# Kernel optimization log

Measured on AMD Instinct MI355X. Metric: run time of the kernel, lower is better.

The kernel has to match this reference:

```python
import jax, jax.numpy as jnp
import numpy as np

EPS = 1e-5
NORM_EPS = 1e-12  # torch F.normalize eps
HEADS = 8


def _ln(x, w, b):
    # channel LayerNorm on NCHW: normalize over C (axis 1), population var
    mu = x.mean(axis=1, keepdims=True)
    var = x.var(axis=1, keepdims=True)
    return (x - mu) / jnp.sqrt(var + EPS) * w[None, :, None, None] + b[None, :, None, None]


def _conv1x1(x, w):
    # x: (B,C,H,W), w: (O,C)
    return jnp.einsum('bchw,oc->bohw', x, w)


def _dwconv3x3(x, w):
    # depthwise 3x3, w: (C,1,3,3)
    C = x.shape[1]
    return jax.lax.conv_general_dilated(
        x, w, window_strides=(1, 1), padding='SAME',
        feature_group_count=C, dimension_numbers=('NCHW', 'OIHW', 'NCHW'))


def _l2norm(v):
    n = jnp.linalg.norm(v, axis=-1, keepdims=True)
    return v / jnp.maximum(n, NORM_EPS)


def setup_inputs() -> dict:
    key = jax.random.key(0)
    ks = jax.random.split(key, 12)
    dim, hid = 128, 512  # hidden_dim = dim * 4
    B, H, W = 8, 128, 128
    s = 0.05
    return {
        'x': jax.random.normal(ks[0], (B, dim, H, W), jnp.float32),
        'ln1_w': jnp.ones((dim,), jnp.float32),
        'ln1_b': jnp.zeros((dim,), jnp.float32),
        'wq': jax.random.normal(ks[1], (dim, dim), jnp.float32) * s,
        'wk': jax.random.normal(ks[2], (dim, dim), jnp.float32) * s,
        'wv': jax.random.normal(ks[3], (dim, dim), jnp.float32) * s,
        'dwq': jax.random.normal(ks[4], (dim, 1, 3, 3), jnp.float32) * s,
        'dwk': jax.random.normal(ks[5], (dim, 1, 3, 3), jnp.float32) * s,
        'dwv': jax.random.normal(ks[6], (dim, 1, 3, 3), jnp.float32) * s,
        'temp': jnp.ones((HEADS, 1, 1), jnp.float32),
        'wo': jax.random.normal(ks[7], (dim, dim), jnp.float32) * s,
        'ln2_w': jnp.ones((dim,), jnp.float32),
        'ln2_b': jnp.zeros((dim,), jnp.float32),
        'w_in': jax.random.normal(ks[8], (2 * hid, dim), jnp.float32) * s,
        'dw_ffn': jax.random.normal(ks[9], (2 * hid, 1, 3, 3), jnp.float32) * s,
        'w_out': jax.random.normal(ks[10], (dim, hid), jnp.float32) * s,
    }


def reference(x, ln1_w, ln1_b, wq, wk, wv, dwq, dwk, dwv, temp, wo,
              ln2_w, ln2_b, w_in, dw_ffn, w_out):
    B, C, H, W = x.shape
    d = C // HEADS

    # ---- MDTA channel attention ----
    xn = _ln(x, ln1_w, ln1_b)
    q = _dwconv3x3(_conv1x1(xn, wq), dwq).reshape(B, HEADS, d, H * W)
    k = _dwconv3x3(_conv1x1(xn, wk), dwk).reshape(B, HEADS, d, H * W)
    v = _dwconv3x3(_conv1x1(xn, wv), dwv).reshape(B, HEADS, d, H * W)
    q = _l2norm(q)
    k = _l2norm(k)
    attn = jnp.einsum('bhdn,bhen->bhde', q, k) * temp[None]  # (B,h,d,d)
    attn = jax.nn.softmax(attn, axis=-1)
    out = jnp.einsum('bhde,bhen->bhdn', attn, v).reshape(B, C, H, W)
    x = x + _conv1x1(out, wo)

    # ---- GEGLU FFN with depthwise conv ----
    yn = _ln(x, ln2_w, ln2_b)
    y = _dwconv3x3(_conv1x1(yn, w_in), dw_ffn)
    y1, y2 = jnp.split(y, 2, axis=1)
    y = jax.nn.gelu(y1, approximate=False) * y2
    return x + _conv1x1(y, w_out)
```

## Files before the change

### kernel.cpp

```cpp
#include <hip/hip_runtime.h>
#include <hip/hip_bf16.h>
#include <type_traits>

using bf16 = __hip_bfloat16;
using f32x4  = __attribute__((ext_vector_type(4))) float;
using bf16x8 = __attribute__((ext_vector_type(8))) short;

constexpr int NPIX = 16384;
constexpr int CDIM = 128;

constexpr size_t OFF_MU    = 0;
constexpr size_t OFF_RSTD  = 524288;
constexpr size_t OFF_MU2   = 1048576;
constexpr size_t OFF_RSTD2 = 1572864;
constexpr size_t OFF_SSQ   = 2097152;
constexpr size_t OFF_S     = 2105344;
constexpr size_t OFF_DWP   = 2170880;
constexpr size_t OFF_WQKVB = 2184704;
constexpr size_t OFF_WINB  = 2283008;
constexpr size_t OFF_WOUTB = 2545152;
constexpr size_t OFF_WEFFB = 2676224;
constexpr size_t OFF_X2B   = 2938368;
constexpr size_t OFF_QKV   = 36492800;
constexpr size_t OFF_QKVDW = 137156096;
constexpr size_t OFF_G     = 36492800;
constexpr size_t OFF_Y     = 170710528;

__device__ inline float ldf(const float* p) { return *p; }
__device__ inline float ldf(const bf16* p) { return __bfloat162float(*p); }

__global__ void pack_w(const float* __restrict__ wq, const float* __restrict__ wk,
                       const float* __restrict__ wv, const float* __restrict__ dwq,
                       const float* __restrict__ dwk, const float* __restrict__ dwv,
                       const float* __restrict__ w_in, const float* __restrict__ wout,
                       bf16* __restrict__ Wqkvb, float* __restrict__ dwp,
                       bf16* __restrict__ winb, bf16* __restrict__ woutb) {
    int i = blockIdx.x * 256 + threadIdx.x;
    if (i < 384 * 128) {
        int r = i >> 7, c = i & 127;
        float v = (r < 128) ? wq[r * 128 + c] : (r < 256) ? wk[(r - 128) * 128 + c]
                                                          : wv[(r - 256) * 128 + c];
        Wqkvb[i] = __float2bfloat16(v);
    }
    if (i < 384 * 9) {
        int r = i / 9, j = i % 9;
        dwp[i] = (r < 128) ? dwq[r * 9 + j] : (r < 256) ? dwk[(r - 128) * 9 + j]
                                                        : dwv[(r - 256) * 9 + j];
    }
    if (i < 1024 * 128) winb[i] = __float2bfloat16(w_in[i]);
    if (i < 128 * 512)  woutb[i] = __float2bfloat16(wout[i]);
}

template <typename XT>
__global__ __launch_bounds__(256) void ln_stats(const XT* __restrict__ X, size_t xBs,
                                                float* __restrict__ mu,
                                                float* __restrict__ rstd) {
    const int b = blockIdx.y;
    const XT* Xb = X + (size_t)b * xBs;
    int n = blockIdx.x * 256 + threadIdx.x;
    float s = 0.f, s2 = 0.f;
    for (int c = 0; c < CDIM; ++c) {
        float v = ldf(&Xb[(size_t)c * NPIX + n]);
        s += v; s2 += v * v;
    }
    float m = s * (1.f / CDIM);
    float var = s2 * (1.f / CDIM) - m * m;
    mu[b * NPIX + n] = m;
    rstd[b * NPIX + n] = rsqrtf(var + 1e-5f);
}

template <typename XT, typename OT, typename RT, bool LN, bool RES>
__global__ __launch_bounds__(256) void gemm_mfma(
    const bf16* __restrict__ Wb0, int wBs, const XT* __restrict__ X0, size_t xBs,
    const float* __restrict__ mu0, const float* __restrict__ rstd0,
    const float* __restrict__ lnw, const float* __restrict__ lnb,
    const RT* __restrict__ res0, size_t rBs, OT* __restrict__ out0, size_t oBs, int K) {
    __shared__ bf16 Wl[64][40];
    __shared__ bf16 Xt[128][40];
    const int t = threadIdx.x;
    const int b = blockIdx.z;
    const bf16* Wb = Wb0 + (size_t)b * wBs;
    const XT* X = X0 + (size_t)b * xBs;
    const RT* res = RES ? res0 + (size_t)b * rBs : nullptr;
    OT* out = out0 + (size_t)b * oBs;
    const float* mu = LN ? mu0 + (size_t)b * NPIX : nullptr;
    const float* rstd = LN ? rstd0 + (size_t)b * NPIX : nullptr;

    const int lane = t & 63, wave = t >> 6;
    const int wm = wave >> 1, wn = wave & 1;
    const int g = lane >> 4, lr = lane & 15;
    const int m0 = blockIdx.x * 64, n0 = blockIdx.y * 128;

    const int sw_row = t >> 2, sw_k8 = (t & 3) * 8;
    const int sx_n = t & 127, sx_kh = t >> 7;

    float x_mu = 0.f, x_rs = 0.f;
    if constexpr (LN) { x_mu = mu[n0 + sx_n]; x_rs = rstd[n0 + sx_n]; }

    f32x4 acc[2][4];
    #pragma unroll
    for (int i = 0; i < 2; ++i)
        #pragma unroll
        for (int j = 0; j < 4; ++j)
            acc[i][j] = (f32x4){0.f, 0.f, 0.f, 0.f};

    for (int kc = 0; kc < K; kc += 32) {
        uint4 wv = *(const uint4*)(Wb + (size_t)(m0 + sw_row) * K + kc + sw_k8);
        *(uint4*)&Wl[sw_row][sw_k8] = wv;
        {
            union { uint4 u[2]; bf16 h[16]; } T;
            const int kb = kc + sx_kh * 16;
            #pragma unroll
            for (int kk = 0; kk < 16; ++kk) {
                float v = ldf(&X[(size_t)(kb + kk) * NPIX + n0 + sx_n]);
                if constexpr (LN) v = (v - x_mu) * x_rs * lnw[kb + kk] + lnb[kb + kk];
                T.h[kk] = __float2bfloat16(v);
            }
            *(uint4*)&Xt[sx_n][sx_kh * 16] = T.u[0];
            *(uint4*)&Xt[sx_n][sx_kh * 16 + 8] = T.u[1];
        }
        __syncthreads();
        bf16x8 af[2], bfr[4];
        #pragma unroll
        for (int i = 0; i < 2; ++i)
            af[i] = *(const bf16x8*)&Wl[wm * 32 + i * 16 + lr][g * 8];
        #pragma unroll
        for (int j = 0; j < 4; ++j)
            bfr[j] = *(const bf16x8*)&Xt[wn * 64 + j * 16 + lr][g * 8];
        #pragma unroll
        for (int i = 0; i < 2; ++i)
            #pragma unroll
            for (int j = 0; j < 4; ++j)
                acc[i][j] = __builtin_amdgcn_mfma_f32_16x16x32_bf16(af[i], bfr[j], acc[i][j], 0, 0, 0);
        __syncthreads();
    }
    #pragma unroll
    for (int i = 0; i < 2; ++i) {
        #pragma unroll
        for (int j = 0; j < 4; ++j) {
            #pragma unroll
            for (int r = 0; r < 4; ++r) {
                int row = m0 + wm * 32 + i * 16 + g * 4 + r;
                int col = n0 + wn * 64 + j * 16 + lr;
                float v = acc[i][j][r];
                if constexpr (RES) v += ldf(&res[(size_t)row * NPIX + col]);
                if constexpr (std::is_same_v<OT, float>)
                    out[(size_t)row * NPIX + col] = v;
                else
                    out[(size_t)row * NPIX + col] = __float2bfloat16(v);
            }
        }
    }
}

__global__ __launch_bounds__(256) void dwconv_qkv(const bf16* __restrict__ in0,
                                                  bf16* __restrict__ out0,
                                                  const float* __restrict__ w9,
                                                  float* __restrict__ ssq0) {
    const int b = blockIdx.y, c = blockIdx.x;
    const bf16* in = in0 + ((size_t)b * 384 + c) * NPIX;
    bf16* out = out0 + ((size_t)b * 384 + c) * NPIX;
    float* ssq = ssq0 + b * 256;
    const int t = threadIdx.x;
    const int lane = t & 63;
    const int tx = t & 15, ty = t >> 4;
    const int x0 = tx * 8, ybase = ty * 8;
    float w[9];
    #pragma unroll
    for (int j = 0; j < 9; ++j) w[j] = w9[c * 9 + j];

    float r[3][10];
    auto loadrow = [&](int yy, float* d) {
        union { uint4 u; bf16 h[8]; } V;
        bool ok = (yy >= 0 && yy <= 127);
        V.u = ok ? *(const uint4*)(in + yy * 128 + x0) : make_uint4(0u, 0u, 0u, 0u);
        #pragma unroll
        for (int j = 0; j < 8; ++j) d[j + 1] = __bfloat162float(V.h[j]);
        float Lv = __shfl(d[8], lane - 1, 64);
        float Rv = __shfl(d[1], lane + 1, 64);
        d[0] = (tx == 0) ? 0.f : Lv;
        d[9] = (tx == 15) ? 0.f : Rv;
    };

    loadrow(ybase - 1, r[0]);
    loadrow(ybase, r[1]);
    float s2 = 0.f;
    #pragma unroll
    for (int j = 0; j < 8; ++j) {
        loadrow(ybase + j + 1, r[(j + 2) % 3]);
        const float* rm = r[j % 3];
        const float* rc = r[(j + 1) % 3];
        const float* rp = r[(j + 2) % 3];
        union { uint4 u; bf16 h[8]; } O;
        #pragma unroll
        for (int p = 0; p < 8; ++p) {
            float a = w[0] * rm[p] + w[1] * rm[p + 1] + w[2] * rm[p + 2]
                    + w[3] * rc[p] + w[4] * rc[p + 1] + w[5] * rc[p + 2]
                    + w[6] * rp[p] + w[7] * rp[p + 1] + w[8] * rp[p + 2];
            s2 = fmaf(a, a, s2);
            O.h[p] = __float2bfloat16(a);
        }
        *(uint4*)(out + (ybase + j) * 128 + x0) = O.u;
    }
    if (c < 256) {
        #pragma unroll
        for (int off = 32; off; off >>= 1) s2 += __shfl_down(s2, off);
        if (lane == 0) atomicAdd(&ssq[c], s2);
    }
}

__global__ __launch_bounds__(256) void attn_scores(const bf16* __restrict__ qkvdw0,
                                                   float* __restrict__ S0) {
    const int b = blockIdx.z;
    const bf16* base = qkvdw0 + (size_t)b * 384 * NPIX;
    float* S = S0 + b * 2048;
    const int h = blockIdx.x;
    const int n00 = blockIdx.y * 2048;
    __shared__ bf16 ql[16][264], kl[16][264];
    __shared__ float sacc[4][256];
    const int t = threadIdx.x;
    const int lane = t & 63, wave = t >> 6;
    const int lr = lane & 15, g = lane >> 4;
    const bf16* qbase = base + (size_t)(h * 16) * NPIX;
    const bf16* kbase = base + (size_t)(128 + h * 16) * NPIX;

    f32x4 acc = (f32x4){0.f, 0.f, 0.f, 0.f};
    for (int it = 0; it < 8; ++it) {
        const int n0 = n00 + it * 256;
        __syncthreads();
        #pragma unroll
        for (int s = 0; s < 2; ++s) {
            int idx = t + s * 256;
            int row = idx >> 5, cc = (idx & 31) * 8;
            *(uint4*)&ql[row][cc] = *(const uint4*)(qbase + (size_t)row * NPIX + n0 + cc);
            *(uint4*)&kl[row][cc] = *(const uint4*)(kbase + (size_t)row * NPIX + n0 + cc);
        }
        __syncthreads();
        #pragma unroll
        for (int m = 0; m < 2; ++m) {
            const int kc = wave * 64 + m * 32 + g * 8;
            bf16x8 aq = *(const bf16x8*)&ql[lr][kc];
            bf16x8 bk = *(const bf16x8*)&kl[lr][kc];
            acc = __builtin_amdgcn_mfma_f32_16x16x32_bf16(aq, bk, acc, 0, 0, 0);
        }
    }
    #pragma unroll
    for (int r = 0; r < 4; ++r) {
        int d = g * 4 + r, e = lr;
        sacc[wave][d * 16 + e] = acc[r];
    }
    __syncthreads();
    float s = sacc[0][t] + sacc[1][t] + sacc[2][t] + sacc[3][t];
    atomicAdd(&S[h * 256 + t], s);
}

__global__ __launch_bounds__(256) void softmax_weff(const float* __restrict__ S0,
                                                    const float* __restrict__ ssq0,
                                                    const float* __restrict__ temp,
                                                    const float* __restrict__ wo,
                                                    bf16* __restrict__ Weffb0) {
    const int b = blockIdx.x;
    const float* S = S0 + b * 2048;
    const float* ssq = ssq0 + b * 256;
    bf16* Weffb = Weffb0 + b * 16384;
    __shared__ float at[2048];
    __shared__ float rn[256];
    int t = threadIdx.x;
    rn[t] = 1.f / fmaxf(sqrtf(ssq[t]), 1e-12f);
    __syncthreads();
    for (int i = t; i < 2048; i += 256) {
        int hd = i >> 4, e = i & 15, h = hd >> 4;
        at[i] = S[i] * rn[hd] * rn[128 + h * 16 + e] * temp[h];
    }
    __syncthreads();
    if (t < 128) {
        float mx = -1e30f;
        for (int e = 0; e < 16; ++e) mx = fmaxf(mx, at[t * 16 + e]);
        float s = 0.f;
        for (int e = 0; e < 16; ++e) { float v = expf(at[t * 16 + e] - mx); at[t * 16 + e] = v; s += v; }
        float inv = 1.f / s;
        for (int e = 0; e < 16; ++e) at[t * 16 + e] *= inv;
    }
    __syncthreads();
    int o = t >> 1, half = t & 1;
    for (int j = 0; j < 64; ++j) {
        int col = half * 64 + j;
        int h16 = col & ~15, e = col & 15;
        float s = 0.f;
        #pragma unroll
        for (int dd = 0; dd < 16; ++dd)
            s = fmaf(wo[o * 128 + h16 + dd], at[(h16 + dd) * 16 + e], s);
        Weffb[o * 128 + col] = __float2bfloat16(s);
    }
}

__global__ __launch_bounds__(256) void geglu_dw(const bf16* __restrict__ g0,
                                                bf16* __restrict__ y0,
                                                const float* __restrict__ dww) {
    const int b = blockIdx.y, c = blockIdx.x;
    const bf16* g1 = g0 + ((size_t)b * 1024 + c) * NPIX;
    const bf16* g2 = g0 + ((size_t)b * 1024 + c + 512) * NPIX;
    bf16* y = y0 + ((size_t)b * 512 + c) * NPIX;
    const int t = threadIdx.x;
    const int lane = t & 63;
    const int tx = t & 15, ty = t >> 4;
    const int x0 = tx * 8, ybase = ty * 8;
    float w1[9], w2[9];
    #pragma unroll
    for (int j = 0; j < 9; ++j) { w1[j] = dww[c * 9 + j]; w2[j] = dww[(c + 512) * 9 + j]; }

    float ra[3][10], rb[3][10];
    auto loadrow = [&](const bf16* src, int yy, float* d) {
        union { uint4 u; bf16 h[8]; } V;
        bool ok = (yy >= 0 && yy <= 127);
        V.u = ok ? *(const uint4*)(src + yy * 128 + x0) : make_uint4(0u, 0u, 0u, 0u);
        #pragma unroll
        for (int j = 0; j < 8; ++j) d[j + 1] = __bfloat162float(V.h[j]);
        float Lv = __shfl(d[8], lane - 1, 64);
        float Rv = __shfl(d[1], lane + 1, 64);
        d[0] = (tx == 0) ? 0.f : Lv;
        d[9] = (tx == 15) ? 0.f : Rv;
    };

    loadrow(g1, ybase - 1, ra[0]); loadrow(g1, ybase, ra[1]);
    loadrow(g2, ybase - 1, rb[0]); loadrow(g2, ybase, rb[1]);
    #pragma unroll
    for (int j = 0; j < 8; ++j) {
        loadrow(g1, ybase + j + 1, ra[(j + 2) % 3]);
        loadrow(g2, ybase + j + 1, rb[(j + 2) % 3]);
        const float* am = ra[j % 3]; const float* ac = ra[(j + 1) % 3]; const float* ap = ra[(j + 2) % 3];
        const float* bm = rb[j % 3]; const float* bc = rb[(j + 1) % 3]; const float* bp = rb[(j + 2) % 3];
        union { uint4 u; bf16 h[8]; } O;
        #pragma unroll
        for (int p = 0; p < 8; ++p) {
            float a1 = w1[0] * am[p] + w1[1] * am[p + 1] + w1[2] * am[p + 2]
                     + w1[3] * ac[p] + w1[4] * ac[p + 1] + w1[5] * ac[p + 2]
                     + w1[6] * ap[p] + w1[7] * ap[p + 1] + w1[8] * ap[p + 2];
            float a2 = w2[0] * bm[p] + w2[1] * bm[p + 1] + w2[2] * bm[p + 2]
                     + w2[3] * bc[p] + w2[4] * bc[p + 1] + w2[5] * bc[p + 2]
                     + w2[6] * bp[p] + w2[7] * bp[p + 1] + w2[8] * bp[p + 2];
            float gelu = 0.5f * a1 * (1.f + erff(a1 * 0.70710678118f));
            O.h[p] = __float2bfloat16(gelu * a2);
        }
        *(uint4*)(y + (ybase + j) * 128 + x0) = O.u;
    }
}

extern "C" void kernel_launch(void* const* d_in, const int* in_sizes, int n_in,
                              void* d_out, int out_size, void* d_ws, size_t ws_size,
                              hipStream_t stream) {
    const float* x    = (const float*)d_in[0];
    const float* ln1w = (const float*)d_in[1];
    const float* ln1b = (const float*)d_in[2];
    const float* wq   = (const float*)d_in[3];
    const float* wk   = (const float*)d_in[4];
    const float* wv   = (const float*)d_in[5];
    const float* dwq  = (const float*)d_in[6];
    const float* dwk  = (const float*)d_in[7];
    const float* dwv  = (const float*)d_in[8];
    const float* temp = (const float*)d_in[9];
    const float* wo   = (const float*)d_in[10];
    const float* ln2w = (const float*)d_in[11];
    const float* ln2b = (const float*)d_in[12];
    const float* w_in = (const float*)d_in[13];
    const float* dwf  = (const float*)d_in[14];
    const float* wout = (const float*)d_in[15];
    float* out = (float*)d_out;
    char* ws = (char*)d_ws;

    float* mu    = (float*)(ws + OFF_MU);
    float* rstd  = (float*)(ws + OFF_RSTD);
    float* mu2   = (float*)(ws + OFF_MU2);
    float* rstd2 = (float*)(ws + OFF_RSTD2);
    float* ssq   = (float*)(ws + OFF_SSQ);
    float* S     = (float*)(ws + OFF_S);
    float* dwp   = (float*)(ws + OFF_DWP);
    bf16*  Wqkvb = (bf16*)(ws + OFF_WQKVB);
    bf16*  winb  = (bf16*)(ws + OFF_WINB);
    bf16*  woutb = (bf16*)(ws + OFF_WOUTB);
    bf16*  Weffb = (bf16*)(ws + OFF_WEFFB);
    bf16*  x2b   = (bf16*)(ws + OFF_X2B);
    bf16*  qkv   = (bf16*)(ws + OFF_QKV);
    bf16*  qkvdw = (bf16*)(ws + OFF_QKVDW);
    bf16*  g     = (bf16*)(ws + OFF_G);
    bf16*  y     = (bf16*)(ws + OFF_Y);

    const size_t XB = (size_t)CDIM * NPIX;
    const size_t QB = (size_t)384 * NPIX;

    hipMemsetAsync(ws + OFF_SSQ, 0, 73728, stream);
    pack_w<<<512, 256, 0, stream>>>(wq, wk, wv, dwq, dwk, dwv, w_in, wout,
                                    Wqkvb, dwp, winb, woutb);

    ln_stats<float><<<dim3(64, 8), 256, 0, stream>>>(x, XB, mu, rstd);
    gemm_mfma<float, bf16, float, true, false><<<dim3(6, 128, 8), 256, 0, stream>>>(
        Wqkvb, 0, x, XB, mu, rstd, ln1w, ln1b, nullptr, 0, qkv, QB, 128);
    dwconv_qkv<<<dim3(384, 8), 256, 0, stream>>>(qkv, qkvdw, dwp, ssq);
    attn_scores<<<dim3(8, 8, 8), 256, 0, stream>>>(qkvdw, S);
    softmax_weff<<<8, 256, 0, stream>>>(S, ssq, temp, wo, Weffb);
    gemm_mfma<bf16, bf16, float, false, true><<<dim3(2, 128, 8), 256, 0, stream>>>(
        Weffb, 16384, qkvdw + (size_t)256 * NPIX, QB, nullptr, nullptr, nullptr, nullptr,
        x, XB, x2b, XB, 128);
    ln_stats<bf16><<<dim3(64, 8), 256, 0, stream>>>(x2b, XB, mu2, rstd2);

    for (int grp = 0; grp < 2; ++grp) {
        const bf16* x2g = x2b + (size_t)grp * 4 * XB;
        gemm_mfma<bf16, bf16, float, true, false><<<dim3(16, 128, 4), 256, 0, stream>>>(
            winb, 0, x2g, XB, mu2 + (size_t)grp * 4 * NPIX, rstd2 + (size_t)grp * 4 * NPIX,
            ln2w, ln2b, nullptr, 0, g, (size_t)1024 * NPIX, 128);
        geglu_dw<<<dim3(512, 4), 256, 0, stream>>>(g, y, dwf);
        gemm_mfma<bf16, float, bf16, false, true><<<dim3(2, 128, 4), 256, 0, stream>>>(
            woutb, 0, y, (size_t)512 * NPIX, nullptr, nullptr, nullptr, nullptr,
            x2g, XB, out + (size_t)grp * 4 * XB, XB, 512);
    }
    (void)in_sizes; (void)n_in; (void)out_size; (void)ws_size;
}
```

Before: 692.7 us.

## Remap GEMM workgroups per XCD and prenormalize LN2 input before FFN GEMM

Workgroup indices in the MFMA GEMM are remapped so that consecutive logical tiles land on the same XCD, improving L2 reuse of the shared X and W tiles across the chiplets. The LN2 normalization is moved out of the w_in GEMM (where it was recomputed 16 times, once per M-block) into a separate elementwise kernel writing normalized bf16 into the y buffer. The pure-bf16 load path skips the float conversion. This adds an extra read and write of a 4-batch activation and reuses the y scratch region, which relies on xn2 being consumed before geglu_dw writes y.

```diff
diff --git a/kernel.cpp b/kernel.cpp
--- a/kernel.cpp
+++ b/kernel.cpp
@@ -69,6 +69,32 @@
     rstd[b * NPIX + n] = rsqrtf(var + 1e-5f);
 }
 
+__global__ __launch_bounds__(256) void ln2norm(const bf16* __restrict__ x2, size_t xBs,
+                                               const float* __restrict__ mu,
+                                               const float* __restrict__ rstd,
+                                               const float* __restrict__ lnw,
+                                               const float* __restrict__ lnb,
+                                               bf16* __restrict__ xn) {
+    const int b = blockIdx.y;
+    const int id = blockIdx.x * 256 + threadIdx.x;
+    const int c = id >> 11, n8 = (id & 2047) * 8;
+    const bf16* src = x2 + (size_t)b * xBs + (size_t)c * NPIX + n8;
+    bf16* dst = xn + (size_t)b * xBs + (size_t)c * NPIX + n8;
+    const float* mup = mu + (size_t)b * NPIX + n8;
+    const float* rsp = rstd + (size_t)b * NPIX + n8;
+    float lw = lnw[c], lb = lnb[c];
+    union { uint4 u; bf16 h[8]; } V, O;
+    V.u = *(const uint4*)src;
+    float4 m0 = *(const float4*)mup, m1 = *(const float4*)(mup + 4);
+    float4 r0 = *(const float4*)rsp, r1 = *(const float4*)(rsp + 4);
+    float mm[8] = {m0.x, m0.y, m0.z, m0.w, m1.x, m1.y, m1.z, m1.w};
+    float rr[8] = {r0.x, r0.y, r0.z, r0.w, r1.x, r1.y, r1.z, r1.w};
+    #pragma unroll
+    for (int j = 0; j < 8; ++j)
+        O.h[j] = __float2bfloat16((__bfloat162float(V.h[j]) - mm[j]) * rr[j] * lw + lb);
+    *(uint4*)dst = O.u;
+}
+
 template <typename XT, typename OT, typename RT, bool LN, bool RES>
 __global__ __launch_bounds__(256) void gemm_mfma(
     const bf16* __restrict__ Wb0, int wBs, const XT* __restrict__ X0, size_t xBs,
@@ -78,7 +104,16 @@
     __shared__ bf16 Wl[64][40];
     __shared__ bf16 Xt[128][40];
     const int t = threadIdx.x;
-    const int b = blockIdx.z;
+
+    const int gx = gridDim.x, gy = gridDim.y;
+    const int nwg = gx * gy * gridDim.z;
+    const int flat = blockIdx.x + gx * (blockIdx.y + gy * blockIdx.z);
+    const int q = nwg >> 3, r8 = nwg & 7;
+    const int xcd = flat & 7, idx = flat >> 3;
+    const int wid = (xcd < r8 ? xcd * (q + 1) : r8 * (q + 1) + (xcd - r8) * q) + idx;
+    const int mb = wid % gx, rest = wid / gx;
+    const int nb = rest % gy, b = rest / gy;
+
     const bf16* Wb = Wb0 + (size_t)b * wBs;
     const XT* X = X0 + (size_t)b * xBs;
     const RT* res = RES ? res0 + (size_t)b * rBs : nullptr;
@@ -89,7 +124,7 @@
     const int lane = t & 63, wave = t >> 6;
     const int wm = wave >> 1, wn = wave & 1;
     const int g = lane >> 4, lr = lane & 15;
-    const int m0 = blockIdx.x * 64, n0 = blockIdx.y * 128;
+    const int m0 = mb * 64, n0 = nb * 128;
 
     const int sw_row = t >> 2, sw_k8 = (t & 3) * 8;
     const int sx_n = t & 127, sx_kh = t >> 7;
@@ -110,11 +145,18 @@
         {
             union { uint4 u[2]; bf16 h[16]; } T;
             const int kb = kc + sx_kh * 16;
-            #pragma unroll
-            for (int kk = 0; kk < 16; ++kk) {
-                float v = ldf(&X[(size_t)(kb + kk) * NPIX + n0 + sx_n]);
-                if constexpr (LN) v = (v - x_mu) * x_rs * lnw[kb + kk] + lnb[kb + kk];
-                T.h[kk] = __float2bfloat16(v);
+            const XT* xp = X + (size_t)kb * NPIX + n0 + sx_n;
+            if constexpr (std::is_same_v<XT, bf16> && !LN) {
+                #pragma unroll
+                for (int kk = 0; kk < 16; ++kk)
+                    T.h[kk] = xp[(size_t)kk * NPIX];
+            } else {
+                #pragma unroll
+                for (int kk = 0; kk < 16; ++kk) {
+                    float v = ldf(&xp[(size_t)kk * NPIX]);
+                    if constexpr (LN) v = (v - x_mu) * x_rs * lnw[kb + kk] + lnb[kb + kk];
+                    T.h[kk] = __float2bfloat16(v);
+                }
             }
             *(uint4*)&Xt[sx_n][sx_kh * 16] = T.u[0];
             *(uint4*)&Xt[sx_n][sx_kh * 16 + 8] = T.u[1];
@@ -384,6 +426,7 @@
     bf16*  qkvdw = (bf16*)(ws + OFF_QKVDW);
     bf16*  g     = (bf16*)(ws + OFF_G);
     bf16*  y     = (bf16*)(ws + OFF_Y);
+    bf16*  xn2   = (bf16*)(ws + OFF_Y);
 
     const size_t XB = (size_t)CDIM * NPIX;
     const size_t QB = (size_t)384 * NPIX;
@@ -405,9 +448,12 @@
 
     for (int grp = 0; grp < 2; ++grp) {
         const bf16* x2g = x2b + (size_t)grp * 4 * XB;
-        gemm_mfma<bf16, bf16, float, true, false><<<dim3(16, 128, 4), 256, 0, stream>>>(
-            winb, 0, x2g, XB, mu2 + (size_t)grp * 4 * NPIX, rstd2 + (size_t)grp * 4 * NPIX,
-            ln2w, ln2b, nullptr, 0, g, (size_t)1024 * NPIX, 128);
+        const float* mu2g = mu2 + (size_t)grp * 4 * NPIX;
+        const float* rs2g = rstd2 + (size_t)grp * 4 * NPIX;
+        ln2norm<<<dim3(1024, 4), 256, 0, stream>>>(x2g, XB, mu2g, rs2g, ln2w, ln2b, xn2);
+        gemm_mfma<bf16, bf16, float, false, false><<<dim3(16, 128, 4), 256, 0, stream>>>(
+            winb, 0, xn2, XB, nullptr, nullptr, nullptr, nullptr, nullptr, 0,
+            g, (size_t)1024 * NPIX, 128);
         geglu_dw<<<dim3(512, 4), 256, 0, stream>>>(g, y, dwf);
         gemm_mfma<bf16, float, bf16, false, true><<<dim3(2, 128, 4), 256, 0, stream>>>(
             woutb, 0, y, (size_t)512 * NPIX, nullptr, nullptr, nullptr, nullptr,
```

Measured after the change: 590.1 us. -14.8%, faster.
